# Optimization experiments

Measured on AMD Instinct MI355X. Metric: run time of the kernel, lower is better.

## Reference

```python
import jax, jax.numpy as jnp
import numpy as np

N_NODES = 100000
N_EDGES = 1600000
D_IN = 128
D_OUT = 128


def setup_inputs() -> dict:
    key = jax.random.key(0)
    k1, k2, k3, k4 = jax.random.split(key, 4)
    x = jax.random.normal(k1, (N_NODES, D_IN), dtype=jnp.float32)
    edge_index = jax.random.randint(k2, (2, N_EDGES), 0, N_NODES, dtype=jnp.int64)
    # PyTorch Linear default init: U(-1/sqrt(fan_in), 1/sqrt(fan_in))
    bound = 1.0 / np.sqrt(D_IN)
    W1 = jax.random.uniform(k3, (D_OUT, D_IN), minval=-bound, maxval=bound, dtype=jnp.float32)
    W2 = jax.random.uniform(k4, (D_OUT, D_IN), minval=-bound, maxval=bound, dtype=jnp.float32)
    return {"x": x, "edge_index": edge_index, "W1": W1, "W2": W2}


def reference(x, edge_index, W1, W2):
    # self transform: [N, D_out]
    self_features = x @ W1.T
    # neighbor transform: [N, D_out]
    neighbor_features = x @ W2.T
    row, col = edge_index[0], edge_index[1]
    # gather by source (col), scatter-add by destination (row)
    aggregated = jax.ops.segment_sum(neighbor_features[col], row, num_segments=x.shape[0])
    return jax.nn.relu(self_features + aggregated)
```

## Files before the change

### kernel.cpp

```cpp
#include <hip/hip_runtime.h>

#define N_NODES 100000
#define DIM 128
#define NBIN 391
#define BINSZ 256
#define NCH 782
#define CHUNK 2048
#define FCAP 24
#define SLOTS (NBIN * FCAP)
#define ENTCAP 4608
#define FSPB 128
#define LSPB 64
#define NGEMM 782

typedef __attribute__((ext_vector_type(8))) short bf16x8;
typedef __attribute__((ext_vector_type(4))) float f32x4;

__device__ __forceinline__ unsigned short f2bf(float f) {
  unsigned u = __builtin_bit_cast(unsigned, f);
  u += 0x7fff + ((u >> 16) & 1);
  return (unsigned short)(u >> 16);
}
__device__ __forceinline__ float bfhi(unsigned u) {
  return __builtin_bit_cast(float, u & 0xffff0000u);
}
__device__ __forceinline__ float bflo(unsigned u) {
  return __builtin_bit_cast(float, u << 16);
}

__global__ __launch_bounds__(256, 4) void fill_kernel(
    const int* __restrict__ rows, const int* __restrict__ cols,
    int* __restrict__ counts, unsigned* __restrict__ binned,
    int* __restrict__ fspillc, int2* __restrict__ fspill, int n_edges,
    const float* __restrict__ W1, const float* __restrict__ W2,
    unsigned short* __restrict__ Wb) {
  const int tid = threadIdx.x;
  if (blockIdx.x >= NCH) {
    const int v = (blockIdx.x - NCH) * 256 + tid;
    const int j = v >> 5, q = v & 31;
    const float* Wrow =
        (j < 128) ? (W1 + (size_t)j * DIM) : (W2 + (size_t)(j - 128) * DIM);
    const float4 val = *(const float4*)(Wrow + 4 * q);
    const unsigned lo = (unsigned)f2bf(val.x) | ((unsigned)f2bf(val.y) << 16);
    const unsigned hi = (unsigned)f2bf(val.z) | ((unsigned)f2bf(val.w) << 16);
    *(uint2*)(Wb + (size_t)j * DIM + 4 * q) = make_uint2(lo, hi);
    return;
  }

  __shared__ unsigned buf[SLOTS];
  __shared__ int lcnt[NBIN];
  __shared__ int fsc;
  const int ch = blockIdx.x;
  for (int i = tid; i < NBIN; i += 256) lcnt[i] = 0;
  if (tid == 0) fsc = 0;
  __syncthreads();

  const int e0 = ch * CHUNK + tid * 8;
  int rv[8], cv[8];
  int nval;
  if (e0 + 8 <= n_edges) {
    *(int4*)&rv[0] = *(const int4*)(rows + e0);
    *(int4*)&rv[4] = *(const int4*)(rows + e0 + 4);
    *(int4*)&cv[0] = *(const int4*)(cols + e0);
    *(int4*)&cv[4] = *(const int4*)(cols + e0 + 4);
    nval = 8;
  } else {
    nval = 0;
    for (int k = 0; k < 8; ++k)
      if (e0 + k < n_edges) {
        rv[nval] = rows[e0 + k];
        cv[nval] = cols[e0 + k];
        ++nval;
      }
  }
  for (int k = 0; k < nval; ++k) {
    const int r = rv[k];
    const int b = r >> 8;
    const unsigned payload = ((unsigned)(r & 255) << 17) | (unsigned)cv[k];
    const int slot = atomicAdd(&lcnt[b], 1);
    if (slot < FCAP) {
      buf[b * FCAP + slot] = payload;
    } else {
      const int sp = atomicAdd(&fsc, 1);
      if (sp < FSPB) fspill[ch * FSPB + sp] = make_int2(r, cv[k]);
    }
  }
  __syncthreads();

  unsigned* dst = binned + (size_t)ch * SLOTS;
  for (int u = tid; u < SLOTS / 4; u += 256) {
    const int b = u / 6;
    const int q = u - b * 6;
    const int cnt = min(lcnt[b], FCAP);
    if (4 * q < cnt)
      *(uint4*)(dst + 4 * u) = *(const uint4*)&buf[4 * u];
  }
  for (int b = tid; b < NBIN; b += 256)
    counts[(size_t)ch * NBIN + b] = min(lcnt[b], FCAP);
  if (tid == 0) fspillc[ch] = min(fsc, FSPB);
}

__global__ __launch_bounds__(256, 2) void gemm_kernel(
    const float* __restrict__ x, const unsigned short* __restrict__ Wb,
    unsigned short* __restrict__ selfb, unsigned short* __restrict__ neigh) {
  __shared__ unsigned short xs[128 * 136];
  const int tid = threadIdx.x;
  const int t = blockIdx.x;
  const int lane = tid & 63;
  const int w = tid >> 6;
  const int nb = t * 128;
  const int quad = lane >> 4;
  const int l15 = lane & 15;

  bf16x8 bfrag[4][4];
#pragma unroll
  for (int nt = 0; nt < 4; ++nt) {
    const int j = w * 64 + nt * 16 + l15;
#pragma unroll
    for (int ks = 0; ks < 4; ++ks)
      bfrag[nt][ks] =
          *(const bf16x8*)(Wb + (size_t)j * DIM + ks * 32 + quad * 8);
  }

#pragma unroll
  for (int half = 0; half < 2; ++half) {
    float4 av[8];
#pragma unroll
    for (int it = 0; it < 8; ++it) {
      const int v = tid + (half * 8 + it) * 256;
      const int m = v >> 5, q = v & 31;
      av[it] = (nb + m < N_NODES)
                   ? *(const float4*)(x + (size_t)(nb + m) * DIM + 4 * q)
                   : make_float4(0.f, 0.f, 0.f, 0.f);
    }
#pragma unroll
    for (int it = 0; it < 8; ++it) {
      const int v = tid + (half * 8 + it) * 256;
      const int m = v >> 5, q = v & 31;
      const unsigned lo =
          (unsigned)f2bf(av[it].x) | ((unsigned)f2bf(av[it].y) << 16);
      const unsigned hi =
          (unsigned)f2bf(av[it].z) | ((unsigned)f2bf(av[it].w) << 16);
      *(uint2*)&xs[m * 136 + 4 * q] = make_uint2(lo, hi);
    }
  }
  __syncthreads();

  f32x4 acc[8][4];
#pragma unroll
  for (int mt = 0; mt < 8; ++mt)
#pragma unroll
    for (int nt = 0; nt < 4; ++nt) acc[mt][nt] = (f32x4){0.f, 0.f, 0.f, 0.f};

#pragma unroll
  for (int ks = 0; ks < 4; ++ks) {
#pragma unroll
    for (int mt = 0; mt < 8; ++mt) {
      const bf16x8 afrag =
          *(const bf16x8*)&xs[(mt * 16 + l15) * 136 + ks * 32 + quad * 8];
#pragma unroll
      for (int nt = 0; nt < 4; ++nt)
        acc[mt][nt] = __builtin_amdgcn_mfma_f32_16x16x32_bf16(
            afrag, bfrag[nt][ks], acc[mt][nt], 0, 0, 0);
    }
  }

#pragma unroll
  for (int h = 0; h < 2; ++h) {
    __syncthreads();
    if ((w >> 1) == h) {
#pragma unroll
      for (int mt = 0; mt < 8; ++mt)
#pragma unroll
        for (int nt = 0; nt < 4; ++nt) {
          const int col = (w & 1) * 64 + nt * 16 + l15;
#pragma unroll
          for (int r = 0; r < 4; ++r)
            xs[(mt * 16 + quad * 4 + r) * 136 + col] = f2bf(acc[mt][nt][r]);
        }
    }
    __syncthreads();
    unsigned short* dst = h ? neigh : selfb;
#pragma unroll
    for (int it = 0; it < 8; ++it) {
      const int v = it * 256 + tid;
      const int row = v >> 4, q = v & 15;
      if (nb + row < N_NODES)
        *(uint4*)(dst + (size_t)(nb + row) * DIM + 8 * q) =
            *(const uint4*)&xs[row * 136 + 8 * q];
    }
  }
}

__global__ __launch_bounds__(1024, 8) void sortagg_kernel(
    const int* __restrict__ counts, const unsigned* __restrict__ binned,
    const unsigned short* __restrict__ neigh,
    const unsigned short* __restrict__ selfb,
    const int* __restrict__ fspillc, const int2* __restrict__ fspill,
    float* __restrict__ out) {
  __shared__ int segc[NCH];
  __shared__ int ssa[NCH];
  __shared__ unsigned entbuf[ENTCAP];
  __shared__ int outb[ENTCAP];
  __shared__ int hist[BINSZ], hsa[BINSZ], cur[BINSZ];
  __shared__ unsigned lspill[LSPB];
  __shared__ int lsc, tot, hasf;

  const int tid = threadIdx.x;
  const int bin = blockIdx.x;

  if (tid == 0) {
    lsc = 0;
    hasf = 0;
  }
  if (tid < BINSZ) hist[tid] = 0;
  for (int i = tid; i < NCH; i += 1024) {
    const int c = counts[(size_t)i * NBIN + bin];
    segc[i] = c;
    ssa[i] = c;
    if (fspillc[i]) atomicOr(&hasf, 1);
  }
  __syncthreads();

  for (int off = 1; off < NCH; off <<= 1) {
    int add = 0;
    if (tid < NCH && tid >= off) add = ssa[tid - off];
    __syncthreads();
    if (tid < NCH && tid >= off) ssa[tid] += add;
    __syncthreads();
  }
  if (tid == 0) tot = min(ssa[NCH - 1], ENTCAP);

  const unsigned* bbase = binned + (size_t)bin * FCAP;
  for (int u = tid; u < NCH * (FCAP / 4); u += 1024) {
    const int ch = u / 6;
    const int q = u - ch * 6;
    const int cnt = segc[ch];
    if (4 * q < cnt) {
      uint4 v4 = *(const uint4*)(bbase + (size_t)ch * SLOTS + 4 * q);
      const int base = ssa[ch] - cnt;
      const unsigned vals[4] = {v4.x, v4.y, v4.z, v4.w};
#pragma unroll
      for (int j = 0; j < 4; ++j) {
        const int slot = 4 * q + j;
        if (slot < cnt) {
          const int pos = base + slot;
          if (pos < ENTCAP) {
            entbuf[pos] = vals[j];
          } else {
            const int sp = atomicAdd(&lsc, 1);
            if (sp < LSPB) lspill[sp] = vals[j];
          }
        }
      }
    }
  }
  __syncthreads();

  if (hasf) {
    for (int bi = tid; bi < NCH; bi += 1024) {
      const int n = min(fspillc[bi], FSPB);
      for (int i = 0; i < n; ++i) {
        const int2 e = fspill[bi * FSPB + i];
        if ((e.x >> 8) == bin) {
          const unsigned pay = ((unsigned)(e.x & 255) << 17) | (unsigned)e.y;
          const int pos = atomicAdd(&tot, 1);
          if (pos < ENTCAP) {
            entbuf[pos] = pay;
          } else {
            const int sp = atomicAdd(&lsc, 1);
            if (sp < LSPB) lspill[sp] = pay;
          }
        }
      }
    }
    __syncthreads();
  }
  const int total = min(tot, ENTCAP);

  for (int i = tid; i < total; i += 1024)
    atomicAdd(&hist[entbuf[i] >> 17], 1);
  __syncthreads();
  if (tid < BINSZ) hsa[tid] = hist[tid];
  __syncthreads();
  for (int off = 1; off < BINSZ; off <<= 1) {
    int add = 0;
    if (tid < BINSZ && tid >= off) add = hsa[tid - off];
    __syncthreads();
    if (tid < BINSZ && tid >= off) hsa[tid] += add;
    __syncthreads();
  }
  if (tid < BINSZ) cur[tid] = hsa[tid] - hist[tid];
  __syncthreads();

  for (int i = tid; i < total; i += 1024) {
    const unsigned p = entbuf[i];
    const int pos = atomicAdd(&cur[p >> 17], 1);
    outb[pos] = (int)(p & 0x1FFFFu);
  }
  __syncthreads();

  const int l = tid & 63;
  const int wv = tid >> 6;
  const unsigned* ng = (const unsigned*)neigh;
  const unsigned* sfp = (const unsigned*)selfb;
  const int nspill = min(lsc, LSPB);

  for (int k = 0; k < 16; ++k) {
    const int nl = wv * 16 + k;
    const int node = (bin << 8) | nl;
    if (node >= N_NODES) break;
    const int deg = hist[nl];
    const int start = hsa[nl] - hist[nl];
    const unsigned s = sfp[(size_t)node * 64 + l];

    float ax = 0.f, ay = 0.f;
    int d = 0;
    for (; d + 8 <= deg; d += 8) {
      unsigned uv[8];
#pragma unroll
      for (int j = 0; j < 8; ++j)
        uv[j] = ng[(size_t)outb[start + d + j] * 64 + l];
#pragma unroll
      for (int j = 0; j < 8; ++j) {
        ax += bflo(uv[j]);
        ay += bfhi(uv[j]);
      }
    }
    const int rem = deg - d;
    if (rem) {
      unsigned uv[8];
      const int cdup = outb[start + d];
#pragma unroll
      for (int j = 0; j < 8; ++j) {
        const int ci = (j < rem) ? outb[start + d + j] : cdup;
        uv[j] = ng[(size_t)ci * 64 + l];
      }
#pragma unroll
      for (int j = 0; j < 8; ++j) {
        if (j < rem) {
          ax += bflo(uv[j]);
          ay += bfhi(uv[j]);
        }
      }
    }

    for (int i = 0; i < nspill; ++i) {
      const unsigned p = lspill[i];
      if ((int)(p >> 17) == nl) {
        const unsigned u = ng[(size_t)(p & 0x1FFFFu) * 64 + l];
        ax += bflo(u);
        ay += bfhi(u);
      }
    }

    float2 o;
    o.x = fmaxf(bflo(s) + ax, 0.f);
    o.y = fmaxf(bfhi(s) + ay, 0.f);
    *(float2*)(out + (size_t)node * DIM + 2 * l) = o;
  }
}

extern "C" void kernel_launch(void* const* d_in, const int* in_sizes, int n_in,
                              void* d_out, int out_size, void* d_ws,
                              size_t ws_size, hipStream_t stream) {
  const float* x = (const float*)d_in[0];
  const int* edge_index = (const int*)d_in[1];
  const float* W1 = (const float*)d_in[2];
  const float* W2 = (const float*)d_in[3];
  float* out = (float*)d_out;

  const int n_edges = in_sizes[1] / 2;
  const int* rows = edge_index;
  const int* cols = edge_index + n_edges;

  char* p = (char*)d_ws;
  unsigned short* selfb = (unsigned short*)p;
  p += (size_t)N_NODES * DIM * 2;
  unsigned short* neigh = (unsigned short*)p;
  p += (size_t)N_NODES * DIM * 2;
  unsigned* binned = (unsigned*)p;
  p += (size_t)NCH * SLOTS * 4;
  int* counts = (int*)p;
  p += (size_t)NCH * NBIN * 4;
  p += (size_t)NBIN * ENTCAP * 4;
  p += (size_t)N_NODES * 4;
  p += (size_t)N_NODES * 4;
  int* fspillc = (int*)p;
  p += 4096;
  int2* fspill = (int2*)p;
  p += (size_t)NCH * FSPB * sizeof(int2);
  p += 4096;
  p += (size_t)NBIN * 256 * sizeof(int2);
  unsigned short* Wb = (unsigned short*)p;

  fill_kernel<<<NCH + 32, 256, 0, stream>>>(rows, cols, counts, binned,
                                            fspillc, fspill, n_edges, W1, W2,
                                            Wb);
  gemm_kernel<<<NGEMM, 256, 0, stream>>>(x, Wb, selfb, neigh);
  sortagg_kernel<<<NBIN, 1024, 0, stream>>>(counts, binned, neigh, selfb,
                                            fspillc, fspill, out);
}
```

Baseline: 217.5 us.

## Split each aggregation bin across two XCD-paired blocks by feature half

The sort-and-aggregate kernel now launches two 512-thread blocks per bin instead of one 1024-thread block. Block IDs are mapped so that the two halves of a bin land on different XCD groups, and each block handles 64 of the 128 output features. Each wave processes two nodes at once, 32 lanes per node, and the fixed-stride loop with a tail branch becomes a single masked gather loop. This doubles the number of blocks and gives the L2 of each XCD group only half the feature columns. The cost is that the binning, scan and sort prologue is redundantly executed twice per bin, and each gather moves 128 bytes per node instead of 256.

New measurement: 254.3 us. +16.9%, slower.

```diff
diff --git a/kernel.cpp b/kernel.cpp
--- a/kernel.cpp
+++ b/kernel.cpp
@@ -192,7 +192,7 @@
   }
 }
 
-__global__ __launch_bounds__(1024, 8) void sortagg_kernel(
+__global__ __launch_bounds__(512, 6) void sortagg_kernel(
     const int* __restrict__ counts, const unsigned* __restrict__ binned,
     const unsigned short* __restrict__ neigh,
     const unsigned short* __restrict__ selfb,
@@ -207,14 +207,18 @@
   __shared__ int lsc, tot, hasf;
 
   const int tid = threadIdx.x;
-  const int bin = blockIdx.x;
+  const int b = blockIdx.x;
+  const int xcd = b & 7;
+  const int half = xcd >> 2;
+  const int bin = (b >> 3) * 4 + (xcd & 3);
+  if (bin >= NBIN) return;
 
   if (tid == 0) {
     lsc = 0;
     hasf = 0;
   }
   if (tid < BINSZ) hist[tid] = 0;
-  for (int i = tid; i < NCH; i += 1024) {
+  for (int i = tid; i < NCH; i += 512) {
     const int c = counts[(size_t)i * NBIN + bin];
     segc[i] = c;
     ssa[i] = c;
@@ -223,16 +227,19 @@
   __syncthreads();
 
   for (int off = 1; off < NCH; off <<= 1) {
-    int add = 0;
-    if (tid < NCH && tid >= off) add = ssa[tid - off];
-    __syncthreads();
-    if (tid < NCH && tid >= off) ssa[tid] += add;
+    int v0 = 0, v1 = 0;
+    if (tid < NCH && tid >= off) v0 = ssa[tid - off];
+    const int t2 = tid + 512;
+    if (t2 < NCH && t2 >= off) v1 = ssa[t2 - off];
+    __syncthreads();
+    if (tid < NCH && tid >= off) ssa[tid] += v0;
+    if (t2 < NCH && t2 >= off) ssa[t2] += v1;
     __syncthreads();
   }
   if (tid == 0) tot = min(ssa[NCH - 1], ENTCAP);
 
   const unsigned* bbase = binned + (size_t)bin * FCAP;
-  for (int u = tid; u < NCH * (FCAP / 4); u += 1024) {
+  for (int u = tid; u < NCH * (FCAP / 4); u += 512) {
     const int ch = u / 6;
     const int q = u - ch * 6;
     const int cnt = segc[ch];
@@ -258,7 +265,7 @@
   __syncthreads();
 
   if (hasf) {
-    for (int bi = tid; bi < NCH; bi += 1024) {
+    for (int bi = tid; bi < NCH; bi += 512) {
       const int n = min(fspillc[bi], FSPB);
       for (int i = 0; i < n; ++i) {
         const int2 e = fspill[bi * FSPB + i];
@@ -278,7 +285,7 @@
   }
   const int total = min(tot, ENTCAP);
 
-  for (int i = tid; i < total; i += 1024)
+  for (int i = tid; i < total; i += 512)
     atomicAdd(&hist[entbuf[i] >> 17], 1);
   __syncthreads();
   if (tid < BINSZ) hsa[tid] = hist[tid];
@@ -293,7 +300,7 @@
   if (tid < BINSZ) cur[tid] = hsa[tid] - hist[tid];
   __syncthreads();
 
-  for (int i = tid; i < total; i += 1024) {
+  for (int i = tid; i < total; i += 512) {
     const unsigned p = entbuf[i];
     const int pos = atomicAdd(&cur[p >> 17], 1);
     outb[pos] = (int)(p & 0x1FFFFu);
@@ -301,44 +308,35 @@
   __syncthreads();
 
   const int l = tid & 63;
+  const int g = l >> 5;
+  const int q = l & 31;
   const int wv = tid >> 6;
   const unsigned* ng = (const unsigned*)neigh;
   const unsigned* sfp = (const unsigned*)selfb;
+  const int hoff = half * 32;
   const int nspill = min(lsc, LSPB);
 
   for (int k = 0; k < 16; ++k) {
-    const int nl = wv * 16 + k;
+    const int nl = wv * 32 + 2 * k + g;
     const int node = (bin << 8) | nl;
-    if (node >= N_NODES) break;
-    const int deg = hist[nl];
-    const int start = hsa[nl] - hist[nl];
-    const unsigned s = sfp[(size_t)node * 64 + l];
+    const bool valid = node < N_NODES;
+    const int deg = valid ? hist[nl] : 0;
+    int start = hsa[nl] - hist[nl];
+    if (start > ENTCAP - 1) start = ENTCAP - 1;
+    const unsigned s = valid ? sfp[(size_t)node * 64 + hoff + q] : 0u;
 
     float ax = 0.f, ay = 0.f;
-    int d = 0;
-    for (; d + 8 <= deg; d += 8) {
+    const int cdup = outb[start];
+    for (int d = 0; d < deg; d += 8) {
       unsigned uv[8];
 #pragma unroll
-      for (int j = 0; j < 8; ++j)
-        uv[j] = ng[(size_t)outb[start + d + j] * 64 + l];
-#pragma unroll
       for (int j = 0; j < 8; ++j) {
-        ax += bflo(uv[j]);
-        ay += bfhi(uv[j]);
-      }
-    }
-    const int rem = deg - d;
-    if (rem) {
-      unsigned uv[8];
-      const int cdup = outb[start + d];
+        const int ci = (d + j < deg) ? outb[start + d + j] : cdup;
+        uv[j] = ng[(size_t)ci * 64 + hoff + q];
+      }
 #pragma unroll
       for (int j = 0; j < 8; ++j) {
-        const int ci = (j < rem) ? outb[start + d + j] : cdup;
-        uv[j] = ng[(size_t)ci * 64 + l];
-      }
-#pragma unroll
-      for (int j = 0; j < 8; ++j) {
-        if (j < rem) {
+        if (d + j < deg) {
           ax += bflo(uv[j]);
           ay += bfhi(uv[j]);
         }
@@ -347,17 +345,19 @@
 
     for (int i = 0; i < nspill; ++i) {
       const unsigned p = lspill[i];
-      if ((int)(p >> 17) == nl) {
-        const unsigned u = ng[(size_t)(p & 0x1FFFFu) * 64 + l];
+      if (valid && (int)(p >> 17) == nl) {
+        const unsigned u = ng[(size_t)(p & 0x1FFFFu) * 64 + hoff + q];
         ax += bflo(u);
         ay += bfhi(u);
       }
     }
 
-    float2 o;
-    o.x = fmaxf(bflo(s) + ax, 0.f);
-    o.y = fmaxf(bfhi(s) + ay, 0.f);
-    *(float2*)(out + (size_t)node * DIM + 2 * l) = o;
+    if (valid) {
+      float2 o;
+      o.x = fmaxf(bflo(s) + ax, 0.f);
+      o.y = fmaxf(bfhi(s) + ay, 0.f);
+      *(float2*)(out + (size_t)node * DIM + half * 64 + 2 * q) = o;
+    }
   }
 }
 
@@ -398,6 +398,6 @@
                                             fspillc, fspill, n_edges, W1, W2,
                                             Wb);
   gemm_kernel<<<NGEMM, 256, 0, stream>>>(x, Wb, selfb, neigh);
-  sortagg_kernel<<<NBIN, 1024, 0, stream>>>(counts, binned, neigh, selfb,
-                                            fspillc, fspill, out);
-}
+  sortagg_kernel<<<784, 512, 0, stream>>>(counts, binned, neigh, selfb,
+                                          fspillc, fspill, out);
+}
```
